# Kernel tuning notes

Measured on AMD Instinct MI355X. Metric: run time of the kernel, lower is better.

Reference implementation:

```python
import jax, jax.numpy as jnp
from jax import lax
import numpy as np

B, S, D = 4096, 120, 256
DIST = 11
HW = DIST + 1  # grid is (HW, HW)
R = 48         # readout_dim
L = 16         # num residual blocks


def setup_inputs() -> dict:
    key = jax.random.key(0)
    ks = jax.random.split(key, 12)
    sc = 0.02
    return {
        "X": jax.random.normal(ks[0], (B, S, D), jnp.float32),
        "P": jax.random.normal(ks[1], (D,), jnp.float32) * sc,
        "conv_w": jax.random.normal(ks[2], (D, D, 2, 2), jnp.float32) * sc,
        "conv_b": jax.random.normal(ks[3], (D,), jnp.float32) * sc,
        "red_w": jax.random.normal(ks[4], (R, D), jnp.float32) * sc,   # 1x1 conv == linear
        "red_b": jax.random.normal(ks[5], (R,), jnp.float32) * sc,
        "res_w1": jax.random.normal(ks[6], (L, R, R), jnp.float32) * sc,
        "res_b1": jax.random.normal(ks[7], (L, R), jnp.float32) * sc,
        "res_w2": jax.random.normal(ks[8], (L, R, R), jnp.float32) * sc,
        "res_b2": jax.random.normal(ks[9], (L, R), jnp.float32) * sc,
        "out_w": jax.random.normal(ks[10], (1, R), jnp.float32) * sc,
        "out_b": jax.random.normal(ks[11], (1,), jnp.float32) * sc,
    }


def reference(X, P, conv_w, conv_b, red_w, red_b, res_w1, res_b1, res_w2, res_b2, out_w, out_b):
    gelu = lambda t: jax.nn.gelu(t, approximate=False)  # torch F.gelu default = exact erf
    # 1) scatter tokens into grid; cells k<S get X[:,k], remaining cells get pad P
    grid = jnp.broadcast_to(P, (B, HW * HW, D))
    grid = grid.at[:, :S, :].set(X)
    grid = grid.reshape(B, HW, HW, D).transpose(0, 3, 1, 2)  # (B, D, H, W)
    # 2) Conv2d(D, D, k=2, s=2) -> (B, D, 6, 6)
    x = lax.conv_general_dilated(grid, conv_w, window_strides=(2, 2), padding="VALID",
                                 dimension_numbers=("NCHW", "OIHW", "NCHW"))
    x = gelu(x + conv_b[None, :, None, None])
    # 3) 1x1 conv D -> R
    x = jnp.einsum("bdhw,rd->brhw", x, red_w) + red_b[None, :, None, None]
    x = gelu(x)
    # 4) global mean pool -> (B, R)
    x = x.mean(axis=(2, 3))
    # 5) L residual blocks via scan over stacked weights
    def block(h, params):
        w1, b1, w2, b2 = params
        y = gelu(h @ w1.T + b1)
        return h + y @ w2.T + b2, None
    x, _ = lax.scan(block, x, (res_w1, res_b1, res_w2, res_b2))
    # 6) final linear -> (B,)
    return (x @ out_w.T + out_b)[:, 0]
```

## Files before the change

### kernel.cpp

```cpp
#include <hip/hip_runtime.h>
#include <hip/hip_bf16.h>

#define SEQ 120
#define CELLS 30
#define RDIM 48
#define BQ 4096
#define MTOT (BQ*CELLS)
#define MAIN_BLOCKS (MTOT/64)

typedef __bf16 bf16x8 __attribute__((ext_vector_type(8)));
typedef float  f32x4  __attribute__((ext_vector_type(4)));

__device__ __forceinline__ float gelu_f(float x){
  return 0.5f * x * (1.0f + erff(x * 0.7071067811865476f));
}
__device__ __forceinline__ bf16x8 pack8(f32x4 a, f32x4 b){
  bf16x8 r;
  r[0]=(__bf16)a[0]; r[1]=(__bf16)a[1]; r[2]=(__bf16)a[2]; r[3]=(__bf16)a[3];
  r[4]=(__bf16)b[0]; r[5]=(__bf16)b[1]; r[6]=(__bf16)b[2]; r[7]=(__bf16)b[3];
  return r;
}

__global__ void prep_kernel(const float* __restrict__ conv_w, const float* __restrict__ conv_b,
                            const float* __restrict__ P,
                            const float* __restrict__ red_w, const float* __restrict__ red_b,
                            const float* __restrict__ res_w1, const float* __restrict__ res_w2,
                            __bf16* __restrict__ W_bt, __bf16* __restrict__ W_red,
                            __bf16* __restrict__ W1p, __bf16* __restrict__ W2p,
                            float* __restrict__ Gpad)
{
  const int b = blockIdx.x, t = threadIdx.x;
  if (b < 256){
    #pragma unroll
    for (int u=0;u<4;u++){
      int k = u*256 + t;
      W_bt[b*1024 + k] = (__bf16)conv_w[b*1024 + (k&255)*4 + (k>>8)];
    }
  } else if (b == 256){
    for (int i=t; i<48*256; i+=256) W_red[i] = (__bf16)red_w[i];
  } else if (b < 273){
    int l = b - 257;
    #pragma unroll
    for (int u=0;u<12;u++){
      int idx = u*256 + t;
      int j = idx >> 6, k = idx & 63;
      W1p[l*3072 + idx] = (k < 48) ? (__bf16)res_w1[(l*48+j)*48 + k] : (__bf16)0.0f;
    }
  } else if (b < 289){
    int l = b - 273;
    #pragma unroll
    for (int u=0;u<12;u++){
      int idx = u*256 + t;
      int j = idx >> 6, k = idx & 63;
      W2p[l*3072 + idx] = (k < 48) ? (__bf16)res_w2[(l*48+j)*48 + k] : (__bf16)0.0f;
    }
  } else {
    __shared__ float tg[256];
    float z = conv_b[t];
    for (int c=0;c<256;c++){
      const float* w = conv_w + t*1024 + c*4;
      z += (w[0]+w[1]+w[2]+w[3]) * P[c];
    }
    tg[t] = gelu_f(z);
    __syncthreads();
    if (t < 48){
      float g = red_b[t];
      for (int o=0;o<256;o++) g += red_w[t*256+o]*tg[o];
      Gpad[t] = gelu_f(g);
    }
  }
}

__global__ __launch_bounds__(256, 3) void main_kernel(
    const float* __restrict__ X, const __bf16* __restrict__ W_bt,
    const float* __restrict__ conv_b, const __bf16* __restrict__ W_red,
    const float* __restrict__ red_b, float* __restrict__ G)
{
  __shared__ __align__(16) char sm[32768];
  const int tid  = threadIdx.x;
  const int lane = tid & 63;
  const int wave = tid >> 6;
  const int lr = lane & 15, lk = lane >> 4;
  const int m0 = blockIdx.x * 64;

  const int rloc = (wave<<2) + (lane>>4);
  const int csrc = (lane&15) ^ (((rloc&7)<<1) | ((rloc>>3)&1));
  const char* rp[4];
  #pragma unroll
  for (int j=0;j<4;j++){
    int m = m0 + j*16 + rloc;
    int bs = m / 30;
    int cs = m - bs*30;
    int ci = cs/6, cj = cs - ci*6;
    rp[j] = (const char*)(X + ((size_t)bs*SEQ + 24*ci + 2*cj)*256) + csrc*16;
  }

  const __bf16* bbase[4];
  #pragma unroll
  for (int ni=0; ni<4; ++ni)
    bbase[ni] = W_bt + (size_t)(wave*64 + ni*16 + lr)*1024 + lk*8;

  f32x4 acc[4][4];
  #pragma unroll
  for (int a=0;a<4;a++)
    #pragma unroll
    for (int b=0;b<4;b++) acc[a][b] = (f32x4){0.f,0.f,0.f,0.f};

  auto STAGE = [&](int s, int d){
    const int goff = (((s>>3)*12 + ((s>>2)&1)) << 10) + ((s&3) << 8);
    #pragma unroll
    for (int j=0;j<4;j++){
      __builtin_amdgcn_global_load_lds(
        (const __attribute__((address_space(1))) void*)(rp[j] + goff),
        (__attribute__((address_space(3))) void*)(sm + d*16384 + (j<<12) + (wave<<10)),
        16, 0, 0);
    }
  };

  STAGE(0, 0);
  STAGE(1, 1);

  for (int s=0; s<16; ++s){
    const int cur = (s&1)*16384;
    asm volatile("s_waitcnt vmcnt(4)" ::: "memory");
    __builtin_amdgcn_s_barrier();
    __builtin_amdgcn_sched_barrier(0);
    #pragma unroll
    for (int ks=0; ks<2; ++ks){
      bf16x8 bv[4];
      #pragma unroll
      for (int ni=0; ni<4; ++ni)
        bv[ni] = *(const bf16x8*)(bbase[ni] + s*64 + ks*32);
      bf16x8 av[4];
      #pragma unroll
      for (int mi=0; mi<4; ++mi){
        const int row = mi*16 + lr;
        const int key = ((row&7)<<5) | ((row&8)<<1);
        const char* base = sm + cur + row*256;
        f32x4 u0 = *(const f32x4*)(base + ((ks*128 + lk*32     ) ^ key));
        f32x4 u1 = *(const f32x4*)(base + ((ks*128 + lk*32 + 16) ^ key));
        av[mi] = pack8(u0,u1);
      }
      #pragma unroll
      for (int mi=0; mi<4; ++mi)
        #pragma unroll
        for (int ni=0; ni<4; ++ni)
          acc[mi][ni] = __builtin_amdgcn_mfma_f32_16x16x32_bf16(av[mi], bv[ni], acc[mi][ni], 0,0,0);
    }
    __builtin_amdgcn_s_barrier();
    __builtin_amdgcn_sched_barrier(0);
    if (s < 14) STAGE(s+2, s&1);
  }

  #pragma unroll
  for (int ni=0; ni<4; ++ni){
    const int col = wave*64 + ni*16 + lr;
    const float cb = conv_b[col];
    #pragma unroll
    for (int mi=0; mi<4; ++mi){
      #pragma unroll
      for (int reg=0; reg<4; ++reg){
        int row = mi*16 + lk*4 + reg;
        float y = gelu_f(acc[mi][ni][reg] + cb);
        *(__bf16*)(sm + ((row*512 + col*2) ^ ((row&7)<<4))) = (__bf16)y;
      }
    }
  }
  __syncthreads();

  f32x4 acc2[3];
  #pragma unroll
  for (int nf=0;nf<3;nf++) acc2[nf] = (f32x4){0.f,0.f,0.f,0.f};
  const int rowY = wave*16 + lr;
  const int keyY = (rowY&7)<<4;
  #pragma unroll
  for (int kk=0; kk<8; ++kk){
    bf16x8 a2 = *(const bf16x8*)(sm + ((rowY*512 + kk*64 + lk*16) ^ keyY));
    #pragma unroll
    for (int nf=0; nf<3; ++nf){
      bf16x8 b2 = *(const bf16x8*)(W_red + (size_t)(nf*16+lr)*256 + kk*32 + lk*8);
      acc2[nf] = __builtin_amdgcn_mfma_f32_16x16x32_bf16(a2, b2, acc2[nf], 0,0,0);
    }
  }
  #pragma unroll
  for (int nf=0; nf<3; ++nf){
    float rb = red_b[nf*16+lr];
    #pragma unroll
    for (int reg=0; reg<4; ++reg){
      int grow = m0 + wave*16 + lk*4 + reg;
      G[(size_t)grow*RDIM + nf*16 + lr] = gelu_f(acc2[nf][reg] + rb);
    }
  }
}

__global__ __launch_bounds__(64) void head_kernel(
    const float* __restrict__ G, const float* __restrict__ Gpad,
    const __bf16* __restrict__ W1p, const __bf16* __restrict__ W2p,
    const float* __restrict__ res_b1, const float* __restrict__ res_b2,
    const float* __restrict__ out_w, const float* __restrict__ out_b,
    float* __restrict__ out)
{
  __shared__ __align__(16) char Hs[16*256];
  __shared__ __align__(16) char Ys[16*256];
  const int t = threadIdx.x;
  const int lr = t & 15, lk = t >> 4;
  const int b0 = blockIdx.x * 16;

  {
    int row = t >> 2, j4 = 12 + (t & 3);
    int off = (row*256 + j4*16) ^ ((row&7)<<5);
    *(f32x4*)(Hs + off) = (f32x4){0,0,0,0};
    *(f32x4*)(Ys + off) = (f32x4){0,0,0,0};
  }

  #pragma unroll
  for (int pp=0; pp<3; ++pp){
    int idx = pp*64 + t;
    int b = idx / 12, j4 = idx - b*12;
    f32x4 s = ((const f32x4*)Gpad)[j4] * 6.0f;
    const float* g = G + ((size_t)(b0+b)*CELLS)*RDIM + j4*4;
    #pragma unroll
    for (int c=0;c<CELLS;c++) s += *(const f32x4*)(g + c*RDIM);
    s *= (1.0f/36.0f);
    *(f32x4*)(Hs + ((b*256 + j4*16) ^ ((b&7)<<5))) = s;
  }
  __syncthreads();

  const int rowA = lr;
  const int keyA = (rowA&7)<<5;
  for (int l=0; l<16; ++l){
    bf16x8 a[2];
    #pragma unroll
    for (int kk=0;kk<2;kk++){
      f32x4 u0 = *(const f32x4*)(Hs + ((rowA*256 + kk*128 + lk*32) ^ keyA));
      f32x4 u1 = *(const f32x4*)(Hs + ((rowA*256 + kk*128 + lk*32 + 16) ^ keyA));
      a[kk] = pack8(u0,u1);
    }
    #pragma unroll
    for (int nf=0; nf<3; ++nf){
      f32x4 acc = (f32x4){0,0,0,0};
      #pragma unroll
      for (int kk=0;kk<2;kk++){
        bf16x8 bw = *(const bf16x8*)(W1p + ((size_t)l*48 + nf*16 + lr)*64 + kk*32 + lk*8);
        acc = __builtin_amdgcn_mfma_f32_16x16x32_bf16(a[kk], bw, acc, 0,0,0);
      }
      float bj = res_b1[l*48 + nf*16 + lr];
      #pragma unroll
      for (int reg=0; reg<4; ++reg){
        int row = lk*4 + reg;
        *(float*)(Ys + ((row*256 + (nf*16+lr)*4) ^ ((row&7)<<5))) = gelu_f(acc[reg] + bj);
      }
    }
    __syncthreads();
    bf16x8 a2[2];
    #pragma unroll
    for (int kk=0;kk<2;kk++){
      f32x4 u0 = *(const f32x4*)(Ys + ((rowA*256 + kk*128 + lk*32) ^ keyA));
      f32x4 u1 = *(const f32x4*)(Ys + ((rowA*256 + kk*128 + lk*32 + 16) ^ keyA));
      a2[kk] = pack8(u0,u1);
    }
    #pragma unroll
    for (int nf=0; nf<3; ++nf){
      f32x4 acc = (f32x4){0,0,0,0};
      #pragma unroll
      for (int kk=0;kk<2;kk++){
        bf16x8 bw = *(const bf16x8*)(W2p + ((size_t)l*48 + nf*16 + lr)*64 + kk*32 + lk*8);
        acc = __builtin_amdgcn_mfma_f32_16x16x32_bf16(a2[kk], bw, acc, 0,0,0);
      }
      float bj = res_b2[l*48 + nf*16 + lr];
      #pragma unroll
      for (int reg=0; reg<4; ++reg){
        int row = lk*4 + reg;
        float* hp = (float*)(Hs + ((row*256 + (nf*16+lr)*4) ^ ((row&7)<<5)));
        *hp += acc[reg] + bj;
      }
    }
    __syncthreads();
  }

  float s = 0.f;
  #pragma unroll
  for (int i=0;i<12;i++){
    int j = lk*12 + i;
    s += *(const float*)(Hs + ((lr*256 + j*4) ^ ((lr&7)<<5))) * out_w[j];
  }
  s += __shfl_xor(s, 16);
  s += __shfl_xor(s, 32);
  if (lk == 0) out[b0 + lr] = s + out_b[0];
}

extern "C" void kernel_launch(void* const* d_in, const int* in_sizes, int n_in,
                              void* d_out, int out_size, void* d_ws, size_t ws_size,
                              hipStream_t stream) {
  const float* X      = (const float*)d_in[0];
  const float* P      = (const float*)d_in[1];
  const float* conv_w = (const float*)d_in[2];
  const float* conv_b = (const float*)d_in[3];
  const float* red_w  = (const float*)d_in[4];
  const float* red_b  = (const float*)d_in[5];
  const float* res_w1 = (const float*)d_in[6];
  const float* res_b1 = (const float*)d_in[7];
  const float* res_w2 = (const float*)d_in[8];
  const float* res_b2 = (const float*)d_in[9];
  const float* out_w  = (const float*)d_in[10];
  const float* out_b  = (const float*)d_in[11];
  float* out = (float*)d_out;

  char* ws = (char*)d_ws;
  __bf16* W_bt  = (__bf16*)(ws);
  __bf16* W_red = (__bf16*)(ws + 524288);
  __bf16* W1p   = (__bf16*)(ws + 548864);
  __bf16* W2p   = (__bf16*)(ws + 647168);
  float*  Gpad  = (float*)(ws + 745472);
  float*  G     = (float*)(ws + 1048576);

  prep_kernel<<<290, 256, 0, stream>>>(conv_w, conv_b, P, red_w, red_b, res_w1, res_w2,
                                       W_bt, W_red, W1p, W2p, Gpad);
  main_kernel<<<MAIN_BLOCKS, 256, 0, stream>>>(X, W_bt, conv_b, W_red, red_b, G);
  head_kernel<<<BQ/16, 64, 0, stream>>>(G, Gpad, W1p, W2p, res_b1, res_b2, out_w, out_b, out);
}
```

Baseline: 289.4 us.

## Enlarge main GEMM tile to 128 rows and stage weights through LDS

The conv GEMM block grows from 64 to 128 output rows, using 8 waves in a 2x4 arrangement. The bf16 weight operand is now loaded asynchronously into swizzled, double-buffered LDS alongside the activation tile, instead of being read per wave straight from global memory. This halves the number of times each weight tile is fetched per output row and removes global-load latency from the inner MFMA loop. In exchange the block needs 128KB of LDS, which limits each CU to one block and lowers occupancy compared with three 32KB blocks before.

```diff
diff --git a/kernel.cpp b/kernel.cpp
--- a/kernel.cpp
+++ b/kernel.cpp
@@ -6,7 +6,7 @@
 #define RDIM 48
 #define BQ 4096
 #define MTOT (BQ*CELLS)
-#define MAIN_BLOCKS (MTOT/64)
+#define MAIN_BLOCKS (MTOT/128)
 
 typedef __bf16 bf16x8 __attribute__((ext_vector_type(8)));
 typedef float  f32x4  __attribute__((ext_vector_type(4)));
@@ -71,34 +71,38 @@
   }
 }
 
-__global__ __launch_bounds__(256, 3) void main_kernel(
+__global__ __launch_bounds__(512, 2) void main_kernel(
     const float* __restrict__ X, const __bf16* __restrict__ W_bt,
     const float* __restrict__ conv_b, const __bf16* __restrict__ W_red,
     const float* __restrict__ red_b, float* __restrict__ G)
 {
-  __shared__ __align__(16) char sm[32768];
+  __shared__ __align__(16) char sm[131072];
   const int tid  = threadIdx.x;
   const int lane = tid & 63;
   const int wave = tid >> 6;
+  const int wm = wave >> 2, wn = wave & 3;
   const int lr = lane & 15, lk = lane >> 4;
-  const int m0 = blockIdx.x * 64;
-
-  const int rloc = (wave<<2) + (lane>>4);
-  const int csrc = (lane&15) ^ (((rloc&7)<<1) | ((rloc>>3)&1));
-  const char* rp[4];
+  const int m0 = blockIdx.x * 128;
+
+  const char* rpA[4];
   #pragma unroll
   for (int j=0;j<4;j++){
-    int m = m0 + j*16 + rloc;
+    int row = (j*8 + wave)*4 + (lane>>4);
+    int m = m0 + row;
     int bs = m / 30;
     int cs = m - bs*30;
     int ci = cs/6, cj = cs - ci*6;
-    rp[j] = (const char*)(X + ((size_t)bs*SEQ + 24*ci + 2*cj)*256) + csrc*16;
-  }
-
-  const __bf16* bbase[4];
-  #pragma unroll
-  for (int ni=0; ni<4; ++ni)
-    bbase[ni] = W_bt + (size_t)(wave*64 + ni*16 + lr)*1024 + lk*8;
+    int key = ((row&7)<<1) | ((row&8)>>3);
+    int chunk = (lane&15) ^ key;
+    rpA[j] = (const char*)(X + ((size_t)bs*SEQ + 24*ci + 2*cj)*256) + chunk*16;
+  }
+  const char* rpB[4];
+  #pragma unroll
+  for (int j=0;j<4;j++){
+    int col = j*64 + wave*8 + (lane>>3);
+    int chunk = (lane&7) ^ (lane>>3);
+    rpB[j] = (const char*)W_bt + (size_t)col*2048 + chunk*16;
+  }
 
   f32x4 acc[4][4];
   #pragma unroll
@@ -111,8 +115,15 @@
     #pragma unroll
     for (int j=0;j<4;j++){
       __builtin_amdgcn_global_load_lds(
-        (const __attribute__((address_space(1))) void*)(rp[j] + goff),
-        (__attribute__((address_space(3))) void*)(sm + d*16384 + (j<<12) + (wave<<10)),
+        (const __attribute__((address_space(1))) void*)(rpA[j] + goff),
+        (__attribute__((address_space(3))) void*)(sm + d*32768 + (j*8 + wave)*1024),
+        16, 0, 0);
+    }
+    #pragma unroll
+    for (int j=0;j<4;j++){
+      __builtin_amdgcn_global_load_lds(
+        (const __attribute__((address_space(1))) void*)(rpB[j] + s*128),
+        (__attribute__((address_space(3))) void*)(sm + 65536 + d*32768 + (j*64 + wave*8)*128),
         16, 0, 0);
     }
   };
@@ -121,22 +132,26 @@
   STAGE(1, 1);
 
   for (int s=0; s<16; ++s){
-    const int cur = (s&1)*16384;
-    asm volatile("s_waitcnt vmcnt(4)" ::: "memory");
+    const int abuf = (s&1)*32768;
+    const int bbuf = 65536 + (s&1)*32768;
+    if (s < 15) asm volatile("s_waitcnt vmcnt(8)" ::: "memory");
+    else        asm volatile("s_waitcnt vmcnt(0)" ::: "memory");
     __builtin_amdgcn_s_barrier();
     __builtin_amdgcn_sched_barrier(0);
     #pragma unroll
     for (int ks=0; ks<2; ++ks){
       bf16x8 bv[4];
       #pragma unroll
-      for (int ni=0; ni<4; ++ni)
-        bv[ni] = *(const bf16x8*)(bbase[ni] + s*64 + ks*32);
+      for (int ni=0; ni<4; ++ni){
+        const int col = wn*64 + ni*16 + lr;
+        bv[ni] = *(const bf16x8*)(sm + bbuf + col*128 + ((ks*64 + lk*16) ^ ((col&7)<<4)));
+      }
       bf16x8 av[4];
       #pragma unroll
       for (int mi=0; mi<4; ++mi){
-        const int row = mi*16 + lr;
+        const int row = wm*64 + mi*16 + lr;
         const int key = ((row&7)<<5) | ((row&8)<<1);
-        const char* base = sm + cur + row*256;
+        const char* base = sm + abuf + row*256;
         f32x4 u0 = *(const f32x4*)(base + ((ks*128 + lk*32     ) ^ key));
         f32x4 u1 = *(const f32x4*)(base + ((ks*128 + lk*32 + 16) ^ key));
         av[mi] = pack8(u0,u1);
@@ -154,13 +169,13 @@
 
   #pragma unroll
   for (int ni=0; ni<4; ++ni){
-    const int col = wave*64 + ni*16 + lr;
+    const int col = wn*64 + ni*16 + lr;
     const float cb = conv_b[col];
     #pragma unroll
     for (int mi=0; mi<4; ++mi){
       #pragma unroll
       for (int reg=0; reg<4; ++reg){
-        int row = mi*16 + lk*4 + reg;
+        int row = wm*64 + mi*16 + lk*4 + reg;
         float y = gelu_f(acc[mi][ni][reg] + cb);
         *(__bf16*)(sm + ((row*512 + col*2) ^ ((row&7)<<4))) = (__bf16)y;
       }
@@ -316,6 +331,6 @@
 
   prep_kernel<<<290, 256, 0, stream>>>(conv_w, conv_b, P, red_w, red_b, res_w1, res_w2,
                                        W_bt, W_red, W1p, W2p, Gpad);
-  main_kernel<<<MAIN_BLOCKS, 256, 0, stream>>>(X, W_bt, conv_b, W_red, red_b, G);
+  main_kernel<<<MAIN_BLOCKS, 512, 0, stream>>>(X, W_bt, conv_b, W_red, red_b, G);
   head_kernel<<<BQ/16, 64, 0, stream>>>(G, Gpad, W1p, W2p, res_b1, res_b2, out_w, out_b, out);
 }
```

Measured after the change: 262.2 us. -9.4%, faster.
